# Kernel optimization log

Measured on AMD Instinct MI355X. Metric: run time of the kernel, lower is better.

## Reference

```python
import jax, jax.numpy as jnp
import numpy as np

N_NODE = 100000
N_EDGE = 500000
IN_DIM = 128
OUT_DIM = 128
ATTN_DIM = 64
N_REL = 200
N_Q = 64


def setup_inputs() -> dict:
    key = jax.random.key(0)
    ks = jax.random.split(key, 24)
    # edge table: columns [r_idx, _, rel, _, tau, sub, obj]
    r_idx = jax.random.randint(ks[0], (N_EDGE,), 0, N_Q, dtype=jnp.int32)
    rel = jax.random.randint(ks[1], (N_EDGE,), 0, 2 * N_REL + 1, dtype=jnp.int32)
    tau = jax.random.randint(ks[2], (N_EDGE,), -1, 366, dtype=jnp.int32)  # -1 -> q_tau fallback
    sub = jax.random.randint(ks[3], (N_EDGE,), 0, N_NODE, dtype=jnp.int32)
    obj = jax.random.randint(ks[4], (N_EDGE,), 0, N_NODE, dtype=jnp.int32)
    zeros = jnp.zeros((N_EDGE,), jnp.int32)
    edges = jnp.stack([r_idx, zeros, rel, zeros, tau, sub, obj], axis=1)

    def lin(k, fan_in, fan_out):
        return jax.random.normal(k, (fan_in, fan_out), jnp.float32) * (1.0 / np.sqrt(fan_in))

    return {
        "q_sub": jax.random.randint(ks[5], (N_Q,), 0, N_NODE, dtype=jnp.int32),
        "q_rel": jax.random.randint(ks[6], (N_Q,), 0, 2 * N_REL + 1, dtype=jnp.int32),
        "q_tau": 180,
        "hidden": jax.random.normal(ks[7], (N_NODE, IN_DIM), jnp.float32),
        "edges": edges,
        "n_node": N_NODE,
        "old_nodes_new_idx": jax.random.randint(ks[8], (1000,), 0, N_NODE, dtype=jnp.int32),
        "rela_embed": jax.random.normal(ks[9], (2 * N_REL + 1, IN_DIM), jnp.float32),
        "Ws_w": lin(ks[10], IN_DIM, ATTN_DIM),
        "Wr_w": lin(ks[11], IN_DIM, ATTN_DIM),
        "Wqr_w": lin(ks[12], IN_DIM, ATTN_DIM),
        "Wqr_b": jnp.zeros((ATTN_DIM,), jnp.float32),
        "Wtau_w": lin(ks[13], IN_DIM, ATTN_DIM),
        "w_alpha_w": lin(ks[14], ATTN_DIM, 1),
        "w_alpha_b": jnp.zeros((1,), jnp.float32),
        "W_h_w": lin(ks[15], IN_DIM, OUT_DIM),
        "W_h_s_w": lin(ks[16], IN_DIM, OUT_DIM),
        "weight_t1": jax.random.normal(ks[17], (1, IN_DIM), jnp.float32),
        "bias_t1": jax.random.normal(ks[18], (1, IN_DIM), jnp.float32),
        "weight_t2": jax.random.normal(ks[19], (1, IN_DIM), jnp.float32),
        "bias_t2": jax.random.normal(ks[20], (1, IN_DIM), jnp.float32),
    }


def reference(q_sub, q_rel, q_tau, hidden, edges, n_node, old_nodes_new_idx,
              rela_embed, Ws_w, Wr_w, Wqr_w, Wqr_b, Wtau_w,
              w_alpha_w, w_alpha_b, W_h_w, W_h_s_w,
              weight_t1, bias_t1, weight_t2, bias_t2):
    sub = edges[:, 5]
    rel = edges[:, 2]
    obj = edges[:, 6]
    tau = edges[:, 4]
    r_idx = edges[:, 0]

    hs = hidden[sub]                       # [E, in_dim] gather
    hr = rela_embed[rel]                   # [E, in_dim]
    h_qr = rela_embed[q_rel][r_idx]        # [E, in_dim]

    tau = jnp.where(tau >= 0, tau, q_tau)
    delta = (tau - q_tau).astype(hidden.dtype)[:, None]  # [E, 1]
    h_tau = weight_t1 * delta + bias_t1 + jnp.sin(weight_t2 * delta + bias_t2)

    message = hs + hr + h_tau              # [E, in_dim]

    attn = jax.nn.relu(hs @ Ws_w + hr @ Wr_w + (h_qr @ Wqr_w + Wqr_b) + h_tau @ Wtau_w)
    alpha = jax.nn.sigmoid(attn @ w_alpha_w + w_alpha_b)  # [E, 1]

    msg = alpha * message
    msg_s = (1.0 - alpha) * message

    agg = jax.ops.segment_sum(msg, obj, num_segments=n_node)      # [n_node, in_dim]
    agg_s = jax.ops.segment_sum(msg_s, obj, num_segments=n_node)

    hidden_new = agg @ W_h_w       # act is identity (default lambda x: x)
    hidden_new_s = agg_s @ W_h_s_w
    return hidden_new, hidden_new_s
```

## Files before the change

### kernel.cpp

```cpp
#include <hip/hip_runtime.h>
#include <math.h>

#define N_NODE   100000
#define N_EDGE   500000
#define IN_DIM   128
#define OUT_DIM  128
#define ATTN_DIM 64
#define N_RELTAB 401
#define N_QRY    64
#define N_TAU    366

#define SCAN_BLK     256
#define N_SCAN_BLKS  ((N_NODE + SCAN_BLK - 1) / SCAN_BLK)

#define NB_TABLES    (N_TAU + N_RELTAB + N_QRY + 3)
#define NB_COUNT     ((N_EDGE + 255) / 256)
#define NB_NODE      ((N_NODE + 63) / 64)

typedef unsigned int  uint;
typedef unsigned short ushort;
typedef __attribute__((ext_vector_type(8))) short bf16x8;
typedef __attribute__((ext_vector_type(4))) float f32x4;

__device__ __forceinline__ float bfl(uint u)  { return __uint_as_float(u << 16); }
__device__ __forceinline__ float bfh(uint u)  { return __uint_as_float(u & 0xFFFF0000u); }
__device__ __forceinline__ uint  f2bfbits(float f) {
    uint u = __float_as_uint(f);
    return (u + 0x7FFFu + ((u >> 16) & 1u)) >> 16;
}
__device__ __forceinline__ uint  pack2(float lo, float hi) {
    return f2bfbits(lo) | (f2bfbits(hi) << 16);
}

__global__ __launch_bounds__(256) void build_count(const int* __restrict__ q_rel,
                             const int* __restrict__ q_tau_p,
                             const float* __restrict__ rela_embed,
                             const float* __restrict__ Wr_w,
                             const float* __restrict__ Wqr_w,
                             const float* __restrict__ Wqr_b,
                             const float* __restrict__ Wtau_w,
                             const float* __restrict__ w_t1,
                             const float* __restrict__ b_t1,
                             const float* __restrict__ w_t2,
                             const float* __restrict__ b_t2,
                             const float* __restrict__ W_h_w,
                             const float* __restrict__ W_h_s_w,
                             const float* __restrict__ Ws_w,
                             const int* __restrict__ edges,
                             uint* __restrict__ rel_attn_bf,
                             uint* __restrict__ qr_attn_bf,
                             uint* __restrict__ tau_attn_bf,
                             uint* __restrict__ rel_msg_bf,
                             uint* __restrict__ tau_msg_bf,
                             ushort* __restrict__ wfrag_bf,
                             ushort* __restrict__ wsT_bf,
                             int* __restrict__ count) {
    __shared__ float srow[IN_DIM];
    __shared__ float sattn[ATTN_DIM];
    const int b = blockIdx.x;
    const int t = threadIdx.x;

    if (b >= NB_TABLES) {
        const int e = (b - NB_TABLES) * 256 + t;
        if (e < N_EDGE) {
            const int obj = edges[(size_t)e * 7 + 6];
            atomicAdd(&count[obj], 1);
        }
        return;
    }

    if (b < N_TAU) {
        if (t < 128) {
            const int q_tau = *q_tau_p;
            const float delta = (float)(b - q_tau);
            srow[t] = w_t1[t] * delta + b_t1[t] + sinf(w_t2[t] * delta + b_t2[t]);
        }
        __syncthreads();
        if (t < 64) tau_msg_bf[b * 64 + t] = pack2(srow[2 * t], srow[2 * t + 1]);
        if (t < ATTN_DIM) {
            float acc = 0.f;
            #pragma unroll 8
            for (int d = 0; d < IN_DIM; ++d)
                acc += srow[d] * Wtau_w[d * ATTN_DIM + t];
            sattn[t] = acc;
        }
        __syncthreads();
        if (t < 32) tau_attn_bf[b * 32 + t] = pack2(sattn[2 * t], sattn[2 * t + 1]);
    } else if (b < N_TAU + N_RELTAB) {
        const int r = b - N_TAU;
        if (t < 128) srow[t] = rela_embed[r * IN_DIM + t];
        __syncthreads();
        if (t < 64) rel_msg_bf[r * 64 + t] = pack2(srow[2 * t], srow[2 * t + 1]);
        if (t < ATTN_DIM) {
            float acc = 0.f;
            #pragma unroll 8
            for (int d = 0; d < IN_DIM; ++d)
                acc += srow[d] * Wr_w[d * ATTN_DIM + t];
            sattn[t] = acc;
        }
        __syncthreads();
        if (t < 32) rel_attn_bf[r * 32 + t] = pack2(sattn[2 * t], sattn[2 * t + 1]);
    } else if (b < N_TAU + N_RELTAB + N_QRY) {
        const int i = b - N_TAU - N_RELTAB;
        const int r = q_rel[i];
        if (t < 128) srow[t] = rela_embed[r * IN_DIM + t];
        __syncthreads();
        if (t < ATTN_DIM) {
            float acc = Wqr_b[t];
            #pragma unroll 8
            for (int d = 0; d < IN_DIM; ++d)
                acc += srow[d] * Wqr_w[d * ATTN_DIM + t];
            sattn[t] = acc;
        }
        __syncthreads();
        if (t < 32) qr_attn_bf[i * 32 + t] = pack2(sattn[2 * t], sattn[2 * t + 1]);
    } else {
        const int w = b - (N_TAU + N_RELTAB + N_QRY);
        if (w < 2) {
            const float* Wsrc = w ? W_h_s_w : W_h_w;
            ushort* dst = wfrag_bf + (size_t)w * 2048 * 8;
            for (int r = 0; r < 8; ++r) {
                const int s  = t * 8 + r;
                const int ct = s >> 8;
                const int ks = (s >> 6) & 3;
                const int l  = s & 63;
                const int lm = l & 15;
                const int lq = l >> 4;
                union { ushort us[8]; uint4 v; } tmp;
                #pragma unroll
                for (int j = 0; j < 8; ++j)
                    tmp.us[j] = (ushort)f2bfbits(Wsrc[(ks * 32 + lq * 8 + j) * 128 + ct * 16 + lm]);
                *(uint4*)(dst + (size_t)s * 8) = tmp.v;
            }
        } else {
            if (t < 128)
                for (int n = 0; n < 64; ++n)
                    wsT_bf[n * 128 + t] = (ushort)f2bfbits(Ws_w[t * ATTN_DIM + n]);
        }
    }
}

__global__ __launch_bounds__(256) void node_attn_scan(const float* __restrict__ hidden,
                                                      const ushort* __restrict__ wsT_bf,
                                                      uint* __restrict__ hid_bf_u,
                                                      ushort* __restrict__ A_node,
                                                      const int* __restrict__ count,
                                                      int* __restrict__ partial) {
    __shared__ int slds[SCAN_BLK];

    if (blockIdx.x >= NB_NODE) {
        const int blk = blockIdx.x - NB_NODE;
        const int i = blk * SCAN_BLK + threadIdx.x;
        slds[threadIdx.x] = (i < N_NODE) ? count[i] : 0;
        __syncthreads();
        for (int s = SCAN_BLK / 2; s > 0; s >>= 1) {
            if (threadIdx.x < s) slds[threadIdx.x] += slds[threadIdx.x + s];
            __syncthreads();
        }
        if (threadIdx.x == 0) partial[blk] = slds[0];
        return;
    }

    const int wave = threadIdx.x >> 6;
    const int lane = threadIdx.x & 63;
    const int m    = lane & 15;
    const int quad = lane >> 4;
    const int row0 = blockIdx.x * 64 + wave * 16;
    const int row  = row0 + m;
    const int rowc = min(row, N_NODE - 1);

    const float* hsrc = hidden + (size_t)rowc * IN_DIM;
    ushort* hdst = (ushort*)hid_bf_u + (size_t)rowc * 128;

    bf16x8 afr[4];
    #pragma unroll
    for (int ks = 0; ks < 4; ++ks) {
        const int k0 = ks * 32 + quad * 8;
        const float4 v0 = *(const float4*)(hsrc + k0);
        const float4 v1 = *(const float4*)(hsrc + k0 + 4);
        union { uint u[4]; bf16x8 v; } cvt;
        cvt.u[0] = pack2(v0.x, v0.y);
        cvt.u[1] = pack2(v0.z, v0.w);
        cvt.u[2] = pack2(v1.x, v1.y);
        cvt.u[3] = pack2(v1.z, v1.w);
        afr[ks] = cvt.v;
        if (row < N_NODE) *(bf16x8*)(hdst + k0) = cvt.v;
    }

    f32x4 acc[4] = {};
    #pragma unroll
    for (int ks = 0; ks < 4; ++ks) {
        #pragma unroll
        for (int ct = 0; ct < 4; ++ct) {
            const bf16x8 wfr = *(const bf16x8*)(wsT_bf + (ct * 16 + m) * 128 + ks * 32 + quad * 8);
            acc[ct] = __builtin_amdgcn_mfma_f32_16x16x32_bf16(wfr, afr[ks], acc[ct], 0, 0, 0);
        }
    }

    if (row < N_NODE) {
        #pragma unroll
        for (int ct = 0; ct < 4; ++ct) {
            uint2 pk;
            pk.x = pack2(acc[ct][0], acc[ct][1]);
            pk.y = pack2(acc[ct][2], acc[ct][3]);
            *(uint2*)(A_node + (size_t)row * 64 + ct * 16 + quad * 4) = pk;
        }
    }
}

__global__ __launch_bounds__(512) void scan_partials(const int* __restrict__ partial,
                                                     int* __restrict__ blk_off) {
    __shared__ int lds[512];
    const int t = threadIdx.x;
    lds[t] = (t < N_SCAN_BLKS) ? partial[t] : 0;
    __syncthreads();
    for (int d = 1; d < 512; d <<= 1) {
        int v = (t >= d) ? lds[t - d] : 0;
        __syncthreads();
        lds[t] += v;
        __syncthreads();
    }
    if (t < N_SCAN_BLKS) blk_off[t] = (t == 0) ? 0 : lds[t - 1];
}

__global__ __launch_bounds__(SCAN_BLK) void scan_apply(const int* __restrict__ count,
                                                       const int* __restrict__ blk_off,
                                                       int* __restrict__ off,
                                                       int* __restrict__ cursor) {
    __shared__ int lds[SCAN_BLK];
    const int t = threadIdx.x;
    const int i = blockIdx.x * SCAN_BLK + t;
    const int v = (i < N_NODE) ? count[i] : 0;
    lds[t] = v;
    __syncthreads();
    for (int d = 1; d < SCAN_BLK; d <<= 1) {
        int x = (t >= d) ? lds[t - d] : 0;
        __syncthreads();
        lds[t] += x;
        __syncthreads();
    }
    const int excl = blk_off[blockIdx.x] + lds[t] - v;
    if (i < N_NODE) { off[i] = excl; cursor[i] = excl; }
    if (i == N_NODE - 1) off[N_NODE] = excl + v;
}

__global__ __launch_bounds__(256) void alpha_fill(const int* __restrict__ edges,
                                                  const int* __restrict__ q_tau_p,
                                                  const uint* __restrict__ A_node_bf,
                                                  const uint* __restrict__ rel_attn_bf,
                                                  const uint* __restrict__ qr_attn_bf,
                                                  const uint* __restrict__ tau_attn_bf,
                                                  const float* __restrict__ w_alpha_w,
                                                  const float* __restrict__ w_alpha_b,
                                                  int* __restrict__ cursor,
                                                  int4* __restrict__ recs) {
    const int t = threadIdx.x;
    const int q = t & 3;
    const int e = blockIdx.x * 64 + (t >> 2);
    if (e >= N_EDGE) return;

    const int* ed = edges + (size_t)e * 7;
    const int r_idx = ed[0];
    const int rel   = ed[2];
    const int tau   = ed[4];
    const int sub   = ed[5];
    const int obj   = ed[6];
    const int q_tau = *q_tau_p;
    const int tidx  = (tau >= 0) ? tau : q_tau;

    const uint4*  pa = (const uint4*)(A_node_bf  + (size_t)sub * 32) + q * 2;
    const uint4*  pr = (const uint4*)(rel_attn_bf + rel   * 32) + q * 2;
    const uint4*  pq = (const uint4*)(qr_attn_bf  + r_idx * 32) + q * 2;
    const uint4*  pt = (const uint4*)(tau_attn_bf + tidx  * 32) + q * 2;
    const float4* wv = (const float4*)w_alpha_w + q * 4;

    float acc = 0.f;

#define DOT_UINT(va, vr, vq, vt, wlo, whi) do {                                  \
        const float x0 = bfl(va) + bfl(vr) + bfl(vq) + bfl(vt);                  \
        const float x1 = bfh(va) + bfh(vr) + bfh(vq) + bfh(vt);                  \
        acc = fmaf(fmaxf(x0, 0.f), (wlo), fmaf(fmaxf(x1, 0.f), (whi), acc));     \
    } while (0)

    #pragma unroll
    for (int c = 0; c < 2; ++c) {
        const uint4  ua = pa[c];
        const uint4  ur = pr[c];
        const uint4  uq = pq[c];
        const uint4  ut = pt[c];
        const float4 w0 = wv[c * 2];
        const float4 w1 = wv[c * 2 + 1];
        DOT_UINT(ua.x, ur.x, uq.x, ut.x, w0.x, w0.y);
        DOT_UINT(ua.y, ur.y, uq.y, ut.y, w0.z, w0.w);
        DOT_UINT(ua.z, ur.z, uq.z, ut.z, w1.x, w1.y);
        DOT_UINT(ua.w, ur.w, uq.w, ut.w, w1.z, w1.w);
    }
#undef DOT_UINT

    acc += __shfl_xor(acc, 1, 64);
    acc += __shfl_xor(acc, 2, 64);

    if (q == 0) {
        const float alpha = 1.f / (1.f + __expf(-(acc + w_alpha_b[0])));
        const int pos = atomicAdd(&cursor[obj], 1);
        recs[pos] = make_int4(sub * 64, rel * 64, tidx * 64, __float_as_int(alpha));
    }
}

__global__ __launch_bounds__(256) void agg_gemm(const int* __restrict__ off,
                                                const int4* __restrict__ recs,
                                                const uint* __restrict__ hid_bf,
                                                const uint* __restrict__ rel_msg_bf,
                                                const uint* __restrict__ tau_msg_bf,
                                                const ushort* __restrict__ wfrag,
                                                float* __restrict__ out) {
    __shared__ uint lagg[2 * 16 * 64];

    const int wave = threadIdx.x >> 6;
    const int lane = threadIdx.x & 63;
    const int tile = blockIdx.x * 16;

    #pragma unroll
    for (int k = 0; k < 4; ++k) {
        const int n16 = wave * 4 + k;
        const int n = tile + n16;
        const int j0 = off[n];
        const int j1 = off[n + 1];

        float t0 = 0.f, t1 = 0.f;
        float a0 = 0.f, a1 = 0.f;
        for (int j = j0; j < j1; j += 4) {
            int4 r0 = recs[min(j,     j1 - 1)];
            int4 r1 = recs[min(j + 1, j1 - 1)];
            int4 r2 = recs[min(j + 2, j1 - 1)];
            int4 r3 = recs[min(j + 3, j1 - 1)];

            const uint h0 = hid_bf[(size_t)(uint)r0.x + lane];
            const uint h1 = hid_bf[(size_t)(uint)r1.x + lane];
            const uint h2 = hid_bf[(size_t)(uint)r2.x + lane];
            const uint h3 = hid_bf[(size_t)(uint)r3.x + lane];
            const uint e0 = rel_msg_bf[r0.y + lane];
            const uint e1 = rel_msg_bf[r1.y + lane];
            const uint e2 = rel_msg_bf[r2.y + lane];
            const uint e3 = rel_msg_bf[r3.y + lane];
            const uint u0 = tau_msg_bf[r0.z + lane];
            const uint u1 = tau_msg_bf[r1.z + lane];
            const uint u2 = tau_msg_bf[r2.z + lane];
            const uint u3 = tau_msg_bf[r3.z + lane];

#define ACC_EDGE(hh, ee, uu, rr, idx) do {                                   \
            const bool valid = (j + (idx)) < j1;                             \
            const float al = __int_as_float((rr).w);                        \
            float m0 = bfl(hh) + bfl(ee) + bfl(uu);                          \
            float m1 = bfh(hh) + bfh(ee) + bfh(uu);                          \
            m0 = valid ? m0 : 0.f;                                           \
            m1 = valid ? m1 : 0.f;                                           \
            t0 += m0;  t1 += m1;                                             \
            a0 = fmaf(al, m0, a0);                                           \
            a1 = fmaf(al, m1, a1);                                           \
        } while (0)

            ACC_EDGE(h0, e0, u0, r0, 0);
            ACC_EDGE(h1, e1, u1, r1, 1);
            ACC_EDGE(h2, e2, u2, r2, 2);
            ACC_EDGE(h3, e3, u3, r3, 3);
#undef ACC_EDGE
        }
        const int gw = (((lane >> 2) ^ (n16 & 7)) << 2) | (lane & 3);
        lagg[n16 * 64 + gw]        = pack2(a0, a1);
        lagg[1024 + n16 * 64 + gw] = pack2(t0 - a0, t1 - a1);
    }
    __syncthreads();

    const int half = wave & 1;
    const int ctg  = (wave >> 1) * 4;
    const int m    = lane & 15;
    const int quad = lane >> 4;

    bf16x8 bfrag[4];
    #pragma unroll
    for (int ks = 0; ks < 4; ++ks) {
        const int g = (ks * 4 + quad) ^ (m & 7);
        bfrag[ks] = *(const bf16x8*)&lagg[half * 1024 + m * 64 + g * 4];
    }

    f32x4 acc[4] = {};
    #pragma unroll
    for (int ks = 0; ks < 4; ++ks) {
        #pragma unroll
        for (int c = 0; c < 4; ++c) {
            const bf16x8 wfr = *(const bf16x8*)(wfrag +
                ((size_t)(((half * 8 + ctg + c) * 4 + ks) * 64 + lane)) * 8);
            acc[c] = __builtin_amdgcn_mfma_f32_16x16x32_bf16(wfr, bfrag[ks], acc[c], 0, 0, 0);
        }
    }

    float* O = out + (size_t)half * N_NODE * 128 + (size_t)(tile + m) * 128;
    #pragma unroll
    for (int c = 0; c < 4; ++c)
        *(f32x4*)(O + (ctg + c) * 16 + quad * 4) = acc[c];
}

extern "C" void kernel_launch(void* const* d_in, const int* in_sizes, int n_in,
                              void* d_out, int out_size, void* d_ws, size_t ws_size,
                              hipStream_t stream) {
    const int*   q_rel      = (const int*)d_in[1];
    const int*   q_tau_p    = (const int*)d_in[2];
    const float* hidden     = (const float*)d_in[3];
    const int*   edges      = (const int*)d_in[4];
    const float* rela_embed = (const float*)d_in[7];
    const float* Ws_w       = (const float*)d_in[8];
    const float* Wr_w       = (const float*)d_in[9];
    const float* Wqr_w      = (const float*)d_in[10];
    const float* Wqr_b      = (const float*)d_in[11];
    const float* Wtau_w     = (const float*)d_in[12];
    const float* w_alpha_w  = (const float*)d_in[13];
    const float* w_alpha_b  = (const float*)d_in[14];
    const float* W_h_w      = (const float*)d_in[15];
    const float* W_h_s_w    = (const float*)d_in[16];
    const float* w_t1       = (const float*)d_in[17];
    const float* b_t1       = (const float*)d_in[18];
    const float* w_t2       = (const float*)d_in[19];
    const float* b_t2       = (const float*)d_in[20];

    char* p = (char*)d_ws;
    uint* hid_bf      = (uint*)p;                 p += (size_t)N_NODE * 64 * 4;
    uint* A_node_bf   = (uint*)p;                 p += (size_t)N_NODE * 32 * 4;
    int4* recs        = (int4*)p;                 p += (size_t)N_EDGE * 16;
    uint* rel_attn_bf = (uint*)p;                 p += N_RELTAB * 32 * 4;
    uint* qr_attn_bf  = (uint*)p;                 p += N_QRY * 32 * 4;
    uint* tau_attn_bf = (uint*)p;                 p += N_TAU * 32 * 4;
    uint* rel_msg_bf  = (uint*)p;                 p += N_RELTAB * 64 * 4;
    uint* tau_msg_bf  = (uint*)p;                 p += N_TAU * 64 * 4;
    ushort* wfrag_bf  = (ushort*)p;               p += (size_t)2 * 2048 * 8 * 2;
    ushort* wsT_bf    = (ushort*)p;               p += (size_t)64 * 128 * 2;
    int*  count       = (int*)p;                  p += N_NODE * 4;
    int*  off         = (int*)p;                  p += (N_NODE + 1) * 4;
    int*  cursor      = (int*)p;                  p += N_NODE * 4;
    int*  partial     = (int*)p;                  p += N_SCAN_BLKS * 4;
    int*  blk_off     = (int*)p;                  p += N_SCAN_BLKS * 4;

    hipMemsetAsync(count, 0, (size_t)N_NODE * sizeof(int), stream);

    build_count<<<dim3(NB_TABLES + NB_COUNT), dim3(256), 0, stream>>>(
        q_rel, q_tau_p, rela_embed, Wr_w, Wqr_w, Wqr_b, Wtau_w,
        w_t1, b_t1, w_t2, b_t2, W_h_w, W_h_s_w, Ws_w, edges,
        rel_attn_bf, qr_attn_bf, tau_attn_bf, rel_msg_bf, tau_msg_bf,
        wfrag_bf, wsT_bf, count);

    node_attn_scan<<<dim3(NB_NODE + N_SCAN_BLKS), dim3(256), 0, stream>>>(
        hidden, wsT_bf, hid_bf, (ushort*)A_node_bf, count, partial);

    scan_partials<<<dim3(1), dim3(512), 0, stream>>>(partial, blk_off);
    scan_apply<<<dim3(N_SCAN_BLKS), dim3(SCAN_BLK), 0, stream>>>(count, blk_off, off, cursor);

    alpha_fill<<<dim3((N_EDGE + 63) / 64), dim3(256), 0, stream>>>(
        edges, q_tau_p, A_node_bf, rel_attn_bf, qr_attn_bf, tau_attn_bf,
        w_alpha_w, w_alpha_b, cursor, recs);

    agg_gemm<<<dim3(N_NODE / 16), dim3(256), 0, stream>>>(
        off, recs, hid_bf, rel_msg_bf, tau_msg_bf, wfrag_bf, (float*)d_out);
}
```

Before: 324.2 us.

## Fold partial scan into scan_apply and widen per-lane gathers in aggregation

Drops the single-block scan_partials launch by having each scan_apply block reduce the preceding block partials itself, which removes one kernel launch and one serial dependency. In agg_gemm, each half-wave now handles a different edge and each lane loads 8-byte (4 bf16) chunks, so two edges are gathered per instruction with wider loads. A cross-half shuffle then combines the partial sums before the swizzled LDS store. The cost is redundant partial-sum reads in every scan block and extra shuffles per node.

New measurement: 325.5 us. About the same (+0.4%).

```diff
diff --git a/kernel.cpp b/kernel.cpp
--- a/kernel.cpp
+++ b/kernel.cpp
@@ -208,28 +208,28 @@
     }
 }
 
-__global__ __launch_bounds__(512) void scan_partials(const int* __restrict__ partial,
-                                                     int* __restrict__ blk_off) {
-    __shared__ int lds[512];
-    const int t = threadIdx.x;
-    lds[t] = (t < N_SCAN_BLKS) ? partial[t] : 0;
-    __syncthreads();
-    for (int d = 1; d < 512; d <<= 1) {
-        int v = (t >= d) ? lds[t - d] : 0;
-        __syncthreads();
-        lds[t] += v;
-        __syncthreads();
-    }
-    if (t < N_SCAN_BLKS) blk_off[t] = (t == 0) ? 0 : lds[t - 1];
-}
-
 __global__ __launch_bounds__(SCAN_BLK) void scan_apply(const int* __restrict__ count,
-                                                       const int* __restrict__ blk_off,
+                                                       const int* __restrict__ partial,
                                                        int* __restrict__ off,
                                                        int* __restrict__ cursor) {
     __shared__ int lds[SCAN_BLK];
+    __shared__ int base_s;
     const int t = threadIdx.x;
-    const int i = blockIdx.x * SCAN_BLK + t;
+    const int b = blockIdx.x;
+
+    int s = 0;
+    if (t < b) s += partial[t];
+    if (t + 256 < b) s += partial[t + 256];
+    lds[t] = s;
+    __syncthreads();
+    for (int d = SCAN_BLK / 2; d > 0; d >>= 1) {
+        if (t < d) lds[t] += lds[t + d];
+        __syncthreads();
+    }
+    if (t == 0) base_s = lds[0];
+    __syncthreads();
+
+    const int i = b * SCAN_BLK + t;
     const int v = (i < N_NODE) ? count[i] : 0;
     lds[t] = v;
     __syncthreads();
@@ -239,7 +239,7 @@
         lds[t] += x;
         __syncthreads();
     }
-    const int excl = blk_off[blockIdx.x] + lds[t] - v;
+    const int excl = base_s + lds[t] - v;
     if (i < N_NODE) { off[i] = excl; cursor[i] = excl; }
     if (i == N_NODE - 1) off[N_NODE] = excl + v;
 }
@@ -318,6 +318,8 @@
 
     const int wave = threadIdx.x >> 6;
     const int lane = threadIdx.x & 63;
+    const int h    = lane >> 5;
+    const int c    = lane & 31;
     const int tile = blockIdx.x * 16;
 
     #pragma unroll
@@ -327,48 +329,55 @@
         const int j0 = off[n];
         const int j1 = off[n + 1];
 
-        float t0 = 0.f, t1 = 0.f;
-        float a0 = 0.f, a1 = 0.f;
+        float t0 = 0.f, t1 = 0.f, t2 = 0.f, t3 = 0.f;
+        float a0 = 0.f, a1 = 0.f, a2 = 0.f, a3 = 0.f;
+
         for (int j = j0; j < j1; j += 4) {
-            int4 r0 = recs[min(j,     j1 - 1)];
-            int4 r1 = recs[min(j + 1, j1 - 1)];
-            int4 r2 = recs[min(j + 2, j1 - 1)];
-            int4 r3 = recs[min(j + 3, j1 - 1)];
-
-            const uint h0 = hid_bf[(size_t)(uint)r0.x + lane];
-            const uint h1 = hid_bf[(size_t)(uint)r1.x + lane];
-            const uint h2 = hid_bf[(size_t)(uint)r2.x + lane];
-            const uint h3 = hid_bf[(size_t)(uint)r3.x + lane];
-            const uint e0 = rel_msg_bf[r0.y + lane];
-            const uint e1 = rel_msg_bf[r1.y + lane];
-            const uint e2 = rel_msg_bf[r2.y + lane];
-            const uint e3 = rel_msg_bf[r3.y + lane];
-            const uint u0 = tau_msg_bf[r0.z + lane];
-            const uint u1 = tau_msg_bf[r1.z + lane];
-            const uint u2 = tau_msg_bf[r2.z + lane];
-            const uint u3 = tau_msg_bf[r3.z + lane];
-
-#define ACC_EDGE(hh, ee, uu, rr, idx) do {                                   \
-            const bool valid = (j + (idx)) < j1;                             \
-            const float al = __int_as_float((rr).w);                        \
-            float m0 = bfl(hh) + bfl(ee) + bfl(uu);                          \
-            float m1 = bfh(hh) + bfh(ee) + bfh(uu);                          \
-            m0 = valid ? m0 : 0.f;                                           \
-            m1 = valid ? m1 : 0.f;                                           \
-            t0 += m0;  t1 += m1;                                             \
-            a0 = fmaf(al, m0, a0);                                           \
-            a1 = fmaf(al, m1, a1);                                           \
+            const int eA = j + h;
+            const int eB = j + 2 + h;
+            const int4 rA = recs[min(eA, j1 - 1)];
+            const int4 rB = recs[min(eB, j1 - 1)];
+
+            const uint2 hA = *(const uint2*)(hid_bf     + (uint)rA.x + 2 * c);
+            const uint2 gA = *(const uint2*)(rel_msg_bf + rA.y       + 2 * c);
+            const uint2 uA = *(const uint2*)(tau_msg_bf + rA.z       + 2 * c);
+            const uint2 hB = *(const uint2*)(hid_bf     + (uint)rB.x + 2 * c);
+            const uint2 gB = *(const uint2*)(rel_msg_bf + rB.y       + 2 * c);
+            const uint2 uB = *(const uint2*)(tau_msg_bf + rB.z       + 2 * c);
+
+#define ACC_PAIR(hh, gg, uu, rr, ee) do {                                        \
+            const bool vld = (ee) < j1;                                          \
+            const float al = __int_as_float((rr).w);                             \
+            float m0 = bfl((hh).x) + bfl((gg).x) + bfl((uu).x);                  \
+            float m1 = bfh((hh).x) + bfh((gg).x) + bfh((uu).x);                  \
+            float m2 = bfl((hh).y) + bfl((gg).y) + bfl((uu).y);                  \
+            float m3 = bfh((hh).y) + bfh((gg).y) + bfh((uu).y);                  \
+            m0 = vld ? m0 : 0.f;  m1 = vld ? m1 : 0.f;                           \
+            m2 = vld ? m2 : 0.f;  m3 = vld ? m3 : 0.f;                           \
+            t0 += m0;  t1 += m1;  t2 += m2;  t3 += m3;                           \
+            a0 = fmaf(al, m0, a0);  a1 = fmaf(al, m1, a1);                       \
+            a2 = fmaf(al, m2, a2);  a3 = fmaf(al, m3, a3);                       \
         } while (0)
 
-            ACC_EDGE(h0, e0, u0, r0, 0);
-            ACC_EDGE(h1, e1, u1, r1, 1);
-            ACC_EDGE(h2, e2, u2, r2, 2);
-            ACC_EDGE(h3, e3, u3, r3, 3);
-#undef ACC_EDGE
-        }
-        const int gw = (((lane >> 2) ^ (n16 & 7)) << 2) | (lane & 3);
-        lagg[n16 * 64 + gw]        = pack2(a0, a1);
-        lagg[1024 + n16 * 64 + gw] = pack2(t0 - a0, t1 - a1);
+            ACC_PAIR(hA, gA, uA, rA, eA);
+            ACC_PAIR(hB, gB, uB, rB, eB);
+#undef ACC_PAIR
+        }
+
+        t0 += __shfl_xor(t0, 32, 64);  t1 += __shfl_xor(t1, 32, 64);
+        t2 += __shfl_xor(t2, 32, 64);  t3 += __shfl_xor(t3, 32, 64);
+        a0 += __shfl_xor(a0, 32, 64);  a1 += __shfl_xor(a1, 32, 64);
+        a2 += __shfl_xor(a2, 32, 64);  a3 += __shfl_xor(a3, 32, 64);
+
+        if (h == 0) {
+            const int kx  = n16 & 7;
+            const int idx = (((c >> 1) ^ kx) << 2) | ((2 * c) & 3);
+            uint2 pa, pt;
+            pa.x = pack2(a0, a1);            pa.y = pack2(a2, a3);
+            pt.x = pack2(t0 - a0, t1 - a1);  pt.y = pack2(t2 - a2, t3 - a3);
+            *(uint2*)&lagg[n16 * 64 + idx]        = pa;
+            *(uint2*)&lagg[1024 + n16 * 64 + idx] = pt;
+        }
     }
     __syncthreads();
 
@@ -388,17 +397,17 @@
     #pragma unroll
     for (int ks = 0; ks < 4; ++ks) {
         #pragma unroll
-        for (int c = 0; c < 4; ++c) {
+        for (int cc = 0; cc < 4; ++cc) {
             const bf16x8 wfr = *(const bf16x8*)(wfrag +
-                ((size_t)(((half * 8 + ctg + c) * 4 + ks) * 64 + lane)) * 8);
-            acc[c] = __builtin_amdgcn_mfma_f32_16x16x32_bf16(wfr, bfrag[ks], acc[c], 0, 0, 0);
+                ((size_t)(((half * 8 + ctg + cc) * 4 + ks) * 64 + lane)) * 8);
+            acc[cc] = __builtin_amdgcn_mfma_f32_16x16x32_bf16(wfr, bfrag[ks], acc[cc], 0, 0, 0);
         }
     }
 
     float* O = out + (size_t)half * N_NODE * 128 + (size_t)(tile + m) * 128;
     #pragma unroll
-    for (int c = 0; c < 4; ++c)
-        *(f32x4*)(O + (ctg + c) * 16 + quad * 4) = acc[c];
+    for (int cc = 0; cc < 4; ++cc)
+        *(f32x4*)(O + (ctg + cc) * 16 + quad * 4) = acc[cc];
 }
 
 extern "C" void kernel_launch(void* const* d_in, const int* in_sizes, int n_in,
@@ -451,8 +460,7 @@
     node_attn_scan<<<dim3(NB_NODE + N_SCAN_BLKS), dim3(256), 0, stream>>>(
         hidden, wsT_bf, hid_bf, (ushort*)A_node_bf, count, partial);
 
-    scan_partials<<<dim3(1), dim3(512), 0, stream>>>(partial, blk_off);
-    scan_apply<<<dim3(N_SCAN_BLKS), dim3(SCAN_BLK), 0, stream>>>(count, blk_off, off, cursor);
+    scan_apply<<<dim3(N_SCAN_BLKS), dim3(SCAN_BLK), 0, stream>>>(count, partial, off, cursor);
 
     alpha_fill<<<dim3((N_EDGE + 63) / 64), dim3(256), 0, stream>>>(
         edges, q_tau_p, A_node_bf, rel_attn_bf, qr_attn_bf, tau_attn_bf,
```
